# Optimization experiments

Measured on AMD Instinct MI355X. Metric: run time of the kernel, lower is better.

The kernel has to match this reference:

```python
import jax, jax.numpy as jnp
import numpy as np

B, T, H, V, O = 64, 2048, 8, 1000, 1000


def setup_inputs() -> dict:
    key = jax.random.key(0)
    ks = jax.random.split(key, 9)
    X = jax.random.randint(ks[0], (B, T), 0, V, dtype=jnp.int64)
    lengths = jax.random.randint(ks[1], (B,), 1, T + 1, dtype=jnp.int64)
    lengths = lengths.at[0].set(T)  # ensure max(lengths) == T (static output shape)
    s = 1.0 / np.sqrt(H)
    emb = jax.random.normal(ks[2], (V, H), dtype=jnp.float32)
    W_ih = jax.random.uniform(ks[3], (H, H), jnp.float32, -s, s)
    W_hh = jax.random.uniform(ks[4], (H, H), jnp.float32, -s, s)
    b_ih = jax.random.uniform(ks[5], (H,), jnp.float32, -s, s)
    b_hh = jax.random.uniform(ks[6], (H,), jnp.float32, -s, s)
    W_out = jax.random.uniform(ks[7], (O, H), jnp.float32, -s, s)
    b_out = jax.random.uniform(ks[8], (O,), jnp.float32, -s, s)
    return {"X": X, "lengths": lengths, "emb": emb, "W_ih": W_ih,
            "W_hh": W_hh, "b_ih": b_ih, "b_hh": b_hh,
            "W_out": W_out, "b_out": b_out}


def reference(X, lengths, emb, W_ih, W_hh, b_ih, b_hh, W_out, b_out):
    # Embedding gather: [B, T, H]
    x = emb[X]
    # Precompute input projection once (equivalent to per-step W_ih @ x_t)
    x_proj = jnp.einsum('bth,ih->bti', x, W_ih) + b_ih
    h0 = jnp.zeros((X.shape[0], W_hh.shape[0]), dtype=x.dtype)

    def step(h, xt):
        h = jnp.tanh(xt + h @ W_hh.T + b_hh)
        return h, h

    # scan over time: xs shape [T, B, H]
    _, hs = jax.lax.scan(step, h0, jnp.swapaxes(x_proj, 0, 1))
    out = jnp.swapaxes(hs, 0, 1)  # [B, T, H]
    # pad_packed_sequence semantics: positions >= length are zeroed before Linear
    t_idx = jnp.arange(out.shape[1])
    mask = (t_idx[None, :] < lengths[:, None]).astype(out.dtype)  # [B, T]
    out = out * mask[:, :, None]
    # Output projection: [B, T, O]
    logits = jnp.einsum('bth,oh->bto', out, W_out) + b_out
    return logits, lengths
```

## Files before the change

### kernel.cpp

```cpp
#include <hip/hip_runtime.h>
#include <cstdint>
#include <cstddef>
#include <cstring>

#define Bz 64
#define Tz 2048
#define Hz 8
#define Vz 1000
#define Oz 1000

#define SCALE 2.885390081777927f
#define XPCLAMP 117.0f

typedef float f32x4 __attribute__((ext_vector_type(4)));

__global__ __launch_bounds__(256) void k_xproj(
    const int* __restrict__ X, const int* __restrict__ lengths,
    const float* __restrict__ emb, const float* __restrict__ W_ih,
    const float* __restrict__ b_ih, const float* __restrict__ b_hh,
    float* __restrict__ xpT, float* __restrict__ out_tail,
    int* __restrict__ prog)
{
    int r = blockIdx.x * 256 + threadIdx.x;
    if (r < Bz * Tz) {
        int v = X[r];
        const float4* e4 = (const float4*)(emb + (size_t)v * Hz);
        float4 ea = e4[0], eb = e4[1];
        float res[8];
#pragma unroll
        for (int i = 0; i < 8; ++i) {
            const float* w = W_ih + i * 8;
            float a = b_ih[i] + b_hh[i];
            a = fmaf(ea.x, w[0], a); a = fmaf(ea.y, w[1], a);
            a = fmaf(ea.z, w[2], a); a = fmaf(ea.w, w[3], a);
            a = fmaf(eb.x, w[4], a); a = fmaf(eb.y, w[5], a);
            a = fmaf(eb.z, w[6], a); a = fmaf(eb.w, w[7], a);
            res[i] = fminf(a * SCALE, XPCLAMP);
        }
        int b = r >> 11, t = r & 2047;
#pragma unroll
        for (int q = 0; q < 4; ++q) {
            *(float2*)(xpT + ((size_t)(b * 4 + q) * Tz + t) * 2) =
                make_float2(res[2 * q], res[2 * q + 1]);
        }
    }
    if (r < Bz) out_tail[r] = (float)lengths[r];
    if (prog != nullptr && r < 64) prog[r] = 0;
}

#define QROT(x, CTRL) \
    __int_as_float(__builtin_amdgcn_update_dpp(0, __float_as_int(x), (CTRL), 0xF, 0xF, true))

__device__ __forceinline__ float fast_tanh_pre(float m) {
#if __has_builtin(__builtin_amdgcn_exp2f)
    float e = __builtin_amdgcn_exp2f(m);
#else
    float e = exp2f(m);
#endif
#if __has_builtin(__builtin_amdgcn_rcpf)
    return (e - 1.0f) * __builtin_amdgcn_rcpf(e + 1.0f);
#else
    return (e - 1.0f) / (e + 1.0f);
#endif
}

#define STEP(xx, yy, toff) do { \
    float p1x = QROT(h0, 0x39), p1y = QROT(h1, 0x39); \
    float p2x = QROT(h0, 0x4E), p2y = QROT(h1, 0x4E); \
    float p3x = QROT(h0, 0x93), p3y = QROT(h1, 0x93); \
    float s0a = fmaf(h1, w0[1], fmaf(h0, w0[0], (xx))); \
    float s0b = fmaf(h1, w1[1], fmaf(h0, w1[0], (yy))); \
    float s1a = fmaf(p1y, w0[3], p1x * w0[2]); \
    float s1b = fmaf(p1y, w1[3], p1x * w1[2]); \
    float s2a = fmaf(p2y, w0[5], p2x * w0[4]); \
    float s2b = fmaf(p2y, w1[5], p2x * w1[4]); \
    float s3a = fmaf(p3y, w0[7], p3x * w0[6]); \
    float s3b = fmaf(p3y, w1[7], p3x * w1[6]); \
    h0 = fast_tanh_pre((s0a + s1a) + (s2a + s3a)); \
    h1 = fast_tanh_pre((s0b + s1b) + (s2b + s3b)); \
    *(float2*)(hs_base + (size_t)(toff) * (Bz * Hz)) = make_float2(h0, h1); \
} while (0)

template <bool PUB>
__device__ __forceinline__ void scan_run(
    const float* __restrict__ xpT, const float* __restrict__ W_hh,
    float* __restrict__ hs, int b, int q, int* prog, int wv)
{
    int i0 = 2 * q, i1 = 2 * q + 1;
    float w0[8], w1[8];
#pragma unroll
    for (int r = 0; r < 4; ++r) {
        int jj = ((q + r) & 3) * 2;
        w0[2 * r]     = W_hh[i0 * 8 + jj]     * SCALE;
        w0[2 * r + 1] = W_hh[i0 * 8 + jj + 1] * SCALE;
        w1[2 * r]     = W_hh[i1 * 8 + jj]     * SCALE;
        w1[2 * r + 1] = W_hh[i1 * 8 + jj + 1] * SCALE;
    }

    const float4* xp4 = (const float4*)(xpT + (size_t)(b * 4 + q) * Tz * 2);
    float* hs_base = hs + (size_t)b * Hz + 2 * q;

    float h0 = 0.0f, h1 = 0.0f;
    float4 A0 = xp4[0], A1 = xp4[1], A2 = xp4[2], A3 = xp4[3];
    float4 B0 = xp4[4], B1 = xp4[5], B2 = xp4[6], B3 = xp4[7];

    for (int c = 0; c < Tz / 8; ++c) {
        float4 C0 = xp4[4 * c + 8],  C1 = xp4[4 * c + 9];
        float4 C2 = xp4[4 * c + 10], C3 = xp4[4 * c + 11];
        int t0 = c * 8;
        STEP(A0.x, A0.y, t0 + 0); STEP(A0.z, A0.w, t0 + 1);
        STEP(A1.x, A1.y, t0 + 2); STEP(A1.z, A1.w, t0 + 3);
        STEP(A2.x, A2.y, t0 + 4); STEP(A2.z, A2.w, t0 + 5);
        STEP(A3.x, A3.y, t0 + 6); STEP(A3.z, A3.w, t0 + 7);
        A0 = B0; A1 = B1; A2 = B2; A3 = B3;
        B0 = C0; B1 = C1; B2 = C2; B3 = C3;
        if (PUB && ((c & 31) == 31)) {
            if ((threadIdx.x & 63) == 0)
                __hip_atomic_store(&prog[wv * 16], (c >> 5) + 1,
                                   __ATOMIC_RELEASE, __HIP_MEMORY_SCOPE_AGENT);
        }
    }
}

__global__ __launch_bounds__(64) void k_scan(
    const float* __restrict__ xpT, const float* __restrict__ W_hh,
    float* __restrict__ hs)
{
    int lane = threadIdx.x;
    scan_run<false>(xpT, W_hh, hs, blockIdx.x * 16 + (lane >> 2), lane & 3,
                    nullptr, 0);
}

__global__ __launch_bounds__(256) void k_fused(
    const float* __restrict__ xpT, const float* __restrict__ W_hh,
    float* __restrict__ hs, const int* __restrict__ lengths,
    const float* __restrict__ W_out, const float* __restrict__ b_out,
    float* __restrict__ out, int* __restrict__ prog)
{
    __shared__ float4 sh4[128];
    int tid = threadIdx.x;

    if (blockIdx.x == 0) {
        __builtin_amdgcn_s_setprio(3);
        int lane = tid & 63, wv = tid >> 6;
        scan_run<true>(xpT, W_hh, hs, wv * 16 + (lane >> 2), lane & 3, prog, wv);
        return;
    }

    float w[4][8], bo[4];
    if (tid < Oz / 4) {
#pragma unroll
        for (int k = 0; k < 4; ++k) {
            const float4* wr = (const float4*)(W_out + (size_t)(tid * 4 + k) * 8);
            float4 wa = wr[0], wb = wr[1];
            w[k][0] = wa.x; w[k][1] = wa.y; w[k][2] = wa.z; w[k][3] = wa.w;
            w[k][4] = wb.x; w[k][5] = wb.y; w[k][6] = wb.z; w[k][7] = wb.w;
            bo[k] = b_out[tid * 4 + k];
        }
    }

    for (int t = (int)blockIdx.x - 1; t < Tz; t += 255) {
        int need = (t >> 8) + 1;
        if (tid == 0) {
            for (;;) {
                int m0 = __hip_atomic_load(&prog[0], __ATOMIC_RELAXED,
                                           __HIP_MEMORY_SCOPE_AGENT);
                int m1 = __hip_atomic_load(&prog[16], __ATOMIC_RELAXED,
                                           __HIP_MEMORY_SCOPE_AGENT);
                int m2 = __hip_atomic_load(&prog[32], __ATOMIC_RELAXED,
                                           __HIP_MEMORY_SCOPE_AGENT);
                int m3 = __hip_atomic_load(&prog[48], __ATOMIC_RELAXED,
                                           __HIP_MEMORY_SCOPE_AGENT);
                int mn = min(min(m0, m1), min(m2, m3));
                if (mn >= need) break;
                __builtin_amdgcn_s_sleep(16);
            }
        }
        __syncthreads();

        {
            uint64_t u = __hip_atomic_load(
                (const uint64_t*)hs + (size_t)t * 256 + tid,
                __ATOMIC_RELAXED, __HIP_MEMORY_SCOPE_AGENT);
            float2 v;
            __builtin_memcpy(&v, &u, 8);
            int b = tid >> 2;
            if (t >= lengths[b]) v = make_float2(0.f, 0.f);
            ((float2*)sh4)[tid] = v;
        }
        __syncthreads();

        if (tid < Oz / 4) {
            for (int rr = 0; rr < 64; ++rr) {
                float4 ha = sh4[rr * 2], hb = sh4[rr * 2 + 1];
                float r[4];
#pragma unroll
                for (int k = 0; k < 4; ++k) {
                    float a = bo[k];
                    a = fmaf(ha.x, w[k][0], a); a = fmaf(ha.y, w[k][1], a);
                    a = fmaf(ha.z, w[k][2], a); a = fmaf(ha.w, w[k][3], a);
                    a = fmaf(hb.x, w[k][4], a); a = fmaf(hb.y, w[k][5], a);
                    a = fmaf(hb.z, w[k][6], a); a = fmaf(hb.w, w[k][7], a);
                    r[k] = a;
                }
                f32x4 acc = { r[0], r[1], r[2], r[3] };
                *((f32x4*)(out + ((size_t)rr * Tz + t) * Oz) + tid) = acc;
            }
        }
        __syncthreads();
    }
}

__global__ __launch_bounds__(256) void k_out(
    const float* __restrict__ hs, const int* __restrict__ lengths,
    const float* __restrict__ W_out, const float* __restrict__ b_out,
    float* __restrict__ out)
{
    __shared__ float4 sh4[256];
    int tid = threadIdx.x;
    int t0 = blockIdx.x * 2;

    {
        float4 v = ((const float4*)hs)[(size_t)t0 * 128 + tid];
        int tt = tid >> 7, b = (tid & 127) >> 1;
        if (t0 + tt >= lengths[b]) v = make_float4(0.f, 0.f, 0.f, 0.f);
        sh4[tid] = v;
    }
    __syncthreads();

    if (tid >= Oz / 4) return;

    float w[4][8];
    float bo[4];
#pragma unroll
    for (int k = 0; k < 4; ++k) {
        const float4* wr = (const float4*)(W_out + (size_t)(tid * 4 + k) * 8);
        float4 wa = wr[0], wb = wr[1];
        w[k][0] = wa.x; w[k][1] = wa.y; w[k][2] = wa.z; w[k][3] = wa.w;
        w[k][4] = wb.x; w[k][5] = wb.y; w[k][6] = wb.z; w[k][7] = wb.w;
        bo[k] = b_out[tid * 4 + k];
    }

    for (int rr = 0; rr < 128; ++rr) {
        float4 ha = sh4[rr * 2], hb = sh4[rr * 2 + 1];
        int tt = rr >> 6, b = rr & 63;
        float r[4];
#pragma unroll
        for (int k = 0; k < 4; ++k) {
            float a = bo[k];
            a = fmaf(ha.x, w[k][0], a); a = fmaf(ha.y, w[k][1], a);
            a = fmaf(ha.z, w[k][2], a); a = fmaf(ha.w, w[k][3], a);
            a = fmaf(hb.x, w[k][4], a); a = fmaf(hb.y, w[k][5], a);
            a = fmaf(hb.z, w[k][6], a); a = fmaf(hb.w, w[k][7], a);
            r[k] = a;
        }
        f32x4 acc = { r[0], r[1], r[2], r[3] };
        *((f32x4*)(out + ((size_t)b * Tz + t0 + tt) * Oz) + tid) = acc;
    }
}

extern "C" void kernel_launch(void* const* d_in, const int* in_sizes, int n_in,
                              void* d_out, int out_size, void* d_ws, size_t ws_size,
                              hipStream_t stream)
{
    const int*   X       = (const int*)d_in[0];
    const int*   lengths = (const int*)d_in[1];
    const float* emb     = (const float*)d_in[2];
    const float* W_ih    = (const float*)d_in[3];
    const float* W_hh    = (const float*)d_in[4];
    const float* b_ih    = (const float*)d_in[5];
    const float* b_hh    = (const float*)d_in[6];
    const float* W_out   = (const float*)d_in[7];
    const float* b_out   = (const float*)d_in[8];

    float* out   = (float*)d_out;
    float* xpT   = (float*)d_ws;
    float* hs    = xpT + (size_t)Bz * Tz * Hz;

    float* out_tail = out + (size_t)Bz * Tz * Oz;

    size_t base = (size_t)Bz * Tz * Hz * 4 * 2;
    bool fused = (ws_size >= base + 256);
    int* prog = fused ? (int*)((char*)d_ws + base) : nullptr;

    k_xproj<<<(Bz * Tz + 255) / 256, 256, 0, stream>>>(X, lengths, emb, W_ih,
                                                       b_ih, b_hh, xpT, out_tail,
                                                       prog);
    if (fused) {
        k_fused<<<256, 256, 0, stream>>>(xpT, W_hh, hs, lengths, W_out, b_out,
                                         out, prog);
    } else {
        k_scan<<<Bz / 16, 64, 0, stream>>>(xpT, W_hh, hs);
        k_out<<<Tz / 2, 256, 0, stream>>>(hs, lengths, W_out, b_out, out);
    }
}
```

Baseline: 741.2 us.

## Scan with one hidden unit per lane across eight workgroups

The recurrent scan now gives each lane a single hidden unit (8 lanes per batch row) instead of two, and uses DPP row permutations to exchange the hidden state within 8-lane groups. It is spread over 8 blocks of one wave each rather than one block of four waves, so the scan runs on more compute units. The input projection layout changes to per-unit time-contiguous rows to match, and consumers now poll 8 progress flags. The aim is to shorten the serial dependency chain per step. In exchange each step needs more cross-lane moves, and 8 more blocks are taken away from the output projection.

```diff
diff --git a/kernel.cpp b/kernel.cpp
--- a/kernel.cpp
+++ b/kernel.cpp
@@ -14,11 +14,12 @@
 
 typedef float f32x4 __attribute__((ext_vector_type(4)));
 
+
 __global__ __launch_bounds__(256) void k_xproj(
     const int* __restrict__ X, const int* __restrict__ lengths,
     const float* __restrict__ emb, const float* __restrict__ W_ih,
     const float* __restrict__ b_ih, const float* __restrict__ b_hh,
-    float* __restrict__ xpT, float* __restrict__ out_tail,
+    float* __restrict__ xpJ, float* __restrict__ out_tail,
     int* __restrict__ prog)
 {
     int r = blockIdx.x * 256 + threadIdx.x;
@@ -26,7 +27,7 @@
         int v = X[r];
         const float4* e4 = (const float4*)(emb + (size_t)v * Hz);
         float4 ea = e4[0], eb = e4[1];
-        float res[8];
+        int b = r >> 11, t = r & 2047;
 #pragma unroll
         for (int i = 0; i < 8; ++i) {
             const float* w = W_ih + i * 8;
@@ -35,17 +36,11 @@
             a = fmaf(ea.z, w[2], a); a = fmaf(ea.w, w[3], a);
             a = fmaf(eb.x, w[4], a); a = fmaf(eb.y, w[5], a);
             a = fmaf(eb.z, w[6], a); a = fmaf(eb.w, w[7], a);
-            res[i] = fminf(a * SCALE, XPCLAMP);
-        }
-        int b = r >> 11, t = r & 2047;
-#pragma unroll
-        for (int q = 0; q < 4; ++q) {
-            *(float2*)(xpT + ((size_t)(b * 4 + q) * Tz + t) * 2) =
-                make_float2(res[2 * q], res[2 * q + 1]);
+            xpJ[((size_t)(b * 8 + i)) * Tz + t] = fminf(a * SCALE, XPCLAMP);
         }
     }
     if (r < Bz) out_tail[r] = (float)lengths[r];
-    if (prog != nullptr && r < 64) prog[r] = 0;
+    if (prog != nullptr && r < 128) prog[r] = 0;
 }
 
 #define QROT(x, CTRL) \
@@ -64,75 +59,67 @@
 #endif
 }
 
-#define STEP(xx, yy, toff) do { \
-    float p1x = QROT(h0, 0x39), p1y = QROT(h1, 0x39); \
-    float p2x = QROT(h0, 0x4E), p2y = QROT(h1, 0x4E); \
-    float p3x = QROT(h0, 0x93), p3y = QROT(h1, 0x93); \
-    float s0a = fmaf(h1, w0[1], fmaf(h0, w0[0], (xx))); \
-    float s0b = fmaf(h1, w1[1], fmaf(h0, w1[0], (yy))); \
-    float s1a = fmaf(p1y, w0[3], p1x * w0[2]); \
-    float s1b = fmaf(p1y, w1[3], p1x * w1[2]); \
-    float s2a = fmaf(p2y, w0[5], p2x * w0[4]); \
-    float s2b = fmaf(p2y, w1[5], p2x * w1[4]); \
-    float s3a = fmaf(p3y, w0[7], p3x * w0[6]); \
-    float s3b = fmaf(p3y, w1[7], p3x * w1[6]); \
-    h0 = fast_tanh_pre((s0a + s1a) + (s2a + s3a)); \
-    h1 = fast_tanh_pre((s0b + s1b) + (s2b + s3b)); \
-    *(float2*)(hs_base + (size_t)(toff) * (Bz * Hz)) = make_float2(h0, h1); \
+#define STEP(xx, toff) do { \
+    float g1 = QROT(h, 0xB1); \
+    float g2 = QROT(h, 0x4E); \
+    float g3 = QROT(h, 0x1B); \
+    float m7 = QROT(h, 0x141); \
+    float g6 = QROT(m7, 0xB1); \
+    float g5 = QROT(m7, 0x4E); \
+    float g4 = QROT(m7, 0x1B); \
+    float p0 = fmaf(g1, w[1], fmaf(h, w[0], (xx))); \
+    float p1 = fmaf(g3, w[3], g2 * w[2]); \
+    float p2 = fmaf(g5, w[5], g4 * w[4]); \
+    float p3 = fmaf(m7, w[7], g6 * w[6]); \
+    h = fast_tanh_pre((p0 + p1) + (p2 + p3)); \
+    hsp[(size_t)(toff) * (Bz * Hz)] = h; \
 } while (0)
 
 template <bool PUB>
 __device__ __forceinline__ void scan_run(
-    const float* __restrict__ xpT, const float* __restrict__ W_hh,
-    float* __restrict__ hs, int b, int q, int* prog, int wv)
-{
-    int i0 = 2 * q, i1 = 2 * q + 1;
-    float w0[8], w1[8];
-#pragma unroll
-    for (int r = 0; r < 4; ++r) {
-        int jj = ((q + r) & 3) * 2;
-        w0[2 * r]     = W_hh[i0 * 8 + jj]     * SCALE;
-        w0[2 * r + 1] = W_hh[i0 * 8 + jj + 1] * SCALE;
-        w1[2 * r]     = W_hh[i1 * 8 + jj]     * SCALE;
-        w1[2 * r + 1] = W_hh[i1 * 8 + jj + 1] * SCALE;
-    }
-
-    const float4* xp4 = (const float4*)(xpT + (size_t)(b * 4 + q) * Tz * 2);
-    float* hs_base = hs + (size_t)b * Hz + 2 * q;
-
-    float h0 = 0.0f, h1 = 0.0f;
-    float4 A0 = xp4[0], A1 = xp4[1], A2 = xp4[2], A3 = xp4[3];
-    float4 B0 = xp4[4], B1 = xp4[5], B2 = xp4[6], B3 = xp4[7];
+    const float* __restrict__ xpJ, const float* __restrict__ W_hh,
+    float* __restrict__ hs, int lane, int blk, int* prog)
+{
+    int bb = blk * 8 + (lane >> 3);
+    int i = lane & 7;
+
+    float w[8];
+#pragma unroll
+    for (int r = 0; r < 8; ++r)
+        w[r] = W_hh[i * 8 + (i ^ r)] * SCALE;
+
+    const float4* xp4 = (const float4*)(xpJ + ((size_t)bb * 8 + i) * Tz);
+    float* hsp = hs + (size_t)bb * Hz + i;
+
+    float h = 0.0f;
+    float4 A0 = xp4[0], A1 = xp4[1];
+    float4 B0 = xp4[2], B1 = xp4[3];
 
     for (int c = 0; c < Tz / 8; ++c) {
-        float4 C0 = xp4[4 * c + 8],  C1 = xp4[4 * c + 9];
-        float4 C2 = xp4[4 * c + 10], C3 = xp4[4 * c + 11];
+        float4 C0 = xp4[2 * c + 4], C1 = xp4[2 * c + 5];
         int t0 = c * 8;
-        STEP(A0.x, A0.y, t0 + 0); STEP(A0.z, A0.w, t0 + 1);
-        STEP(A1.x, A1.y, t0 + 2); STEP(A1.z, A1.w, t0 + 3);
-        STEP(A2.x, A2.y, t0 + 4); STEP(A2.z, A2.w, t0 + 5);
-        STEP(A3.x, A3.y, t0 + 6); STEP(A3.z, A3.w, t0 + 7);
-        A0 = B0; A1 = B1; A2 = B2; A3 = B3;
-        B0 = C0; B1 = C1; B2 = C2; B3 = C3;
+        STEP(A0.x, t0 + 0); STEP(A0.y, t0 + 1);
+        STEP(A0.z, t0 + 2); STEP(A0.w, t0 + 3);
+        STEP(A1.x, t0 + 4); STEP(A1.y, t0 + 5);
+        STEP(A1.z, t0 + 6); STEP(A1.w, t0 + 7);
+        A0 = B0; A1 = B1; B0 = C0; B1 = C1;
         if (PUB && ((c & 31) == 31)) {
-            if ((threadIdx.x & 63) == 0)
-                __hip_atomic_store(&prog[wv * 16], (c >> 5) + 1,
+            if (lane == 0)
+                __hip_atomic_store(&prog[blk * 16], (c >> 5) + 1,
                                    __ATOMIC_RELEASE, __HIP_MEMORY_SCOPE_AGENT);
         }
     }
 }
 
 __global__ __launch_bounds__(64) void k_scan(
-    const float* __restrict__ xpT, const float* __restrict__ W_hh,
+    const float* __restrict__ xpJ, const float* __restrict__ W_hh,
     float* __restrict__ hs)
 {
-    int lane = threadIdx.x;
-    scan_run<false>(xpT, W_hh, hs, blockIdx.x * 16 + (lane >> 2), lane & 3,
-                    nullptr, 0);
+    scan_run<false>(xpJ, W_hh, hs, threadIdx.x, blockIdx.x, nullptr);
 }
 
 __global__ __launch_bounds__(256) void k_fused(
-    const float* __restrict__ xpT, const float* __restrict__ W_hh,
+    const float* __restrict__ xpJ, const float* __restrict__ W_hh,
     float* __restrict__ hs, const int* __restrict__ lengths,
     const float* __restrict__ W_out, const float* __restrict__ b_out,
     float* __restrict__ out, int* __restrict__ prog)
@@ -140,10 +127,11 @@
     __shared__ float4 sh4[128];
     int tid = threadIdx.x;
 
-    if (blockIdx.x == 0) {
-        __builtin_amdgcn_s_setprio(3);
-        int lane = tid & 63, wv = tid >> 6;
-        scan_run<true>(xpT, W_hh, hs, wv * 16 + (lane >> 2), lane & 3, prog, wv);
+    if (blockIdx.x < 8) {
+        if (tid < 64) {
+            __builtin_amdgcn_s_setprio(3);
+            scan_run<true>(xpJ, W_hh, hs, tid, (int)blockIdx.x, prog);
+        }
         return;
     }
 
@@ -159,19 +147,17 @@
         }
     }
 
-    for (int t = (int)blockIdx.x - 1; t < Tz; t += 255) {
+    for (int t = (int)blockIdx.x - 8; t < Tz; t += 248) {
         int need = (t >> 8) + 1;
         if (tid == 0) {
             for (;;) {
-                int m0 = __hip_atomic_load(&prog[0], __ATOMIC_RELAXED,
-                                           __HIP_MEMORY_SCOPE_AGENT);
-                int m1 = __hip_atomic_load(&prog[16], __ATOMIC_RELAXED,
-                                           __HIP_MEMORY_SCOPE_AGENT);
-                int m2 = __hip_atomic_load(&prog[32], __ATOMIC_RELAXED,
-                                           __HIP_MEMORY_SCOPE_AGENT);
-                int m3 = __hip_atomic_load(&prog[48], __ATOMIC_RELAXED,
-                                           __HIP_MEMORY_SCOPE_AGENT);
-                int mn = min(min(m0, m1), min(m2, m3));
+                int mn = 0x7fffffff;
+#pragma unroll
+                for (int p = 0; p < 8; ++p) {
+                    int m = __hip_atomic_load(&prog[p * 16], __ATOMIC_RELAXED,
+                                              __HIP_MEMORY_SCOPE_AGENT);
+                    mn = min(mn, m);
+                }
                 if (mn >= need) break;
                 __builtin_amdgcn_s_sleep(16);
             }
@@ -274,23 +260,23 @@
     const float* b_out   = (const float*)d_in[8];
 
     float* out   = (float*)d_out;
-    float* xpT   = (float*)d_ws;
-    float* hs    = xpT + (size_t)Bz * Tz * Hz;
+    float* xpJ   = (float*)d_ws;
+    float* hs    = xpJ + (size_t)Bz * Tz * Hz;
 
     float* out_tail = out + (size_t)Bz * Tz * Oz;
 
     size_t base = (size_t)Bz * Tz * Hz * 4 * 2;
-    bool fused = (ws_size >= base + 256);
+    bool fused = (ws_size >= base + 512);
     int* prog = fused ? (int*)((char*)d_ws + base) : nullptr;
 
     k_xproj<<<(Bz * Tz + 255) / 256, 256, 0, stream>>>(X, lengths, emb, W_ih,
-                                                       b_ih, b_hh, xpT, out_tail,
+                                                       b_ih, b_hh, xpJ, out_tail,
                                                        prog);
     if (fused) {
-        k_fused<<<256, 256, 0, stream>>>(xpT, W_hh, hs, lengths, W_out, b_out,
+        k_fused<<<256, 256, 0, stream>>>(xpJ, W_hh, hs, lengths, W_out, b_out,
                                          out, prog);
     } else {
-        k_scan<<<Bz / 16, 64, 0, stream>>>(xpT, W_hh, hs);
+        k_scan<<<Bz / 8, 64, 0, stream>>>(xpJ, W_hh, hs);
         k_out<<<Tz / 2, 256, 0, stream>>>(hs, lengths, W_out, b_out, out);
     }
 }
```

Result: faster. 650.2 us (-12.3%).
